# Kernel tuning notes

Measured on AMD Instinct MI355X. Metric: run time of the kernel, lower is better.

Reference implementation:

```python
import jax, jax.numpy as jnp
import numpy as np

B, T, IN, H, L, P = 512, 512, 1, 100, 4, 0.5  # batch, seq, input, hidden, layers, dropout


def setup_inputs() -> dict:
    key = jax.random.key(0)
    ks = jax.random.split(key, 12)
    k = 1.0 / np.sqrt(H)  # torch nn.LSTM init scale
    u = lambda kk, shape: jax.random.uniform(kk, shape, jnp.float32, -k, k)
    inp = {
        "x": jax.random.normal(ks[0], (B, T, IN), jnp.float32),
        "W_ih0": u(ks[1], (4 * H, IN)),          # layer 0 input weights
        "W_ih_rest": u(ks[2], (L - 1, 4 * H, H)),  # layers 1..3 input weights
        "W_hh": u(ks[3], (L, 4 * H, H)),
        "b_ih": u(ks[4], (L, 4 * H)),
        "b_hh": u(ks[5], (L, 4 * H)),
        "W_out": u(ks[6], (1, H)),
        "b_out": u(ks[7], (1,)),
        # inter-layer dropout keep-masks (torch applies dropout to outputs of layers 0..L-2)
        "drop_masks": jax.random.bernoulli(ks[8], 1.0 - P, (L - 1, B, T, H)).astype(jnp.float32),
    }
    return inp


def _lstm_layer(seq, Wih, Whh, b):
    # seq: [T, B, in_dim]; returns [T, B, H]. PyTorch gate order: i, f, g, o.
    h0 = jnp.zeros((seq.shape[1], Whh.shape[-1]), seq.dtype)

    def step(carry, xt):
        h, c = carry
        gates = xt @ Wih.T + h @ Whh.T + b  # [B, 4H]
        i, f, g, o = jnp.split(gates, 4, axis=-1)
        c = jax.nn.sigmoid(f) * c + jax.nn.sigmoid(i) * jnp.tanh(g)
        h = jax.nn.sigmoid(o) * jnp.tanh(c)
        return (h, c), h

    _, hs = jax.lax.scan(step, (h0, h0), seq)
    return hs


def reference(x, W_ih0, W_ih_rest, W_hh, b_ih, b_hh, W_out, b_out, drop_masks):
    scale = 1.0 / (1.0 - P)
    seq = jnp.swapaxes(x, 0, 1)  # [T, B, IN] (batch_first -> time-major)
    seq = _lstm_layer(seq, W_ih0, W_hh[0], b_ih[0] + b_hh[0])
    for l in range(1, L):
        seq = seq * (jnp.swapaxes(drop_masks[l - 1], 0, 1) * scale)
        seq = _lstm_layer(seq, W_ih_rest[l - 1], W_hh[l], b_ih[l] + b_hh[l])
    last = seq[-1]  # [B, H] == lstm_out[:, -1]
    return last @ W_out.T + b_out  # [B, 1]
```

## Files before the change

### kernel.cpp

```cpp
#include <hip/hip_runtime.h>
#include <cstdint>
#include <cstddef>

#define BB 512
#define TT 512
#define HH 100
#define G4 400

template<bool IS_L0, bool WRITE_DROP>
__global__ __launch_bounds__(448, 1)
void rec_kernel(const float* __restrict__ x,
                const float* __restrict__ xc,
                const float* __restrict__ Whh_l,
                const float* __restrict__ Wih0,
                const float* __restrict__ bih_l,
                const float* __restrict__ bhh_l,
                const float* __restrict__ dmask_l,
                float* __restrict__ hdrop,
                float* __restrict__ st_h,
                float* __restrict__ st_c)
{
    __shared__ float sh[G4 * HH];

    const int tid  = threadIdx.x;
    const int e    = (tid < 224) ? 0 : 1;
    const int off  = tid - e * 224;
    const int j    = off >> 1;
    const int role = off & 1;
    const bool active = (j < HH);
    const int jc   = active ? j : (HH - 1);
    const int r0   = role * 100 + jc;
    const int r1   = r0 + 200;
    const int b    = blockIdx.x * 2 + e;

    {
        const float4* src = (const float4*)Whh_l;
        float4* dst = (float4*)sh;
        for (int i = tid; i < G4 * HH / 4; i += 448) dst[i] = src[i];
    }
    __syncthreads();

    float4 wf0[25], wf1[25];
    {
        const float4* s0 = (const float4*)&sh[r0 * HH];
        const float4* s1 = (const float4*)&sh[r1 * HH];
        #pragma unroll
        for (int m = 0; m < 25; ++m) { wf0[m] = s0[m]; wf1[m] = s1[m]; }
    }
    __syncthreads();

    for (int i = tid; i < G4 * HH; i += 448) sh[i] = 0.f;

    float wx0 = 0.f, wx1 = 0.f, bs0 = 0.f, bs1 = 0.f;
    if (IS_L0) {
        wx0 = Wih0[r0];  bs0 = bih_l[r0] + bhh_l[r0];
        wx1 = Wih0[r1];  bs1 = bih_l[r1] + bhh_l[r1];
    }

    const bool isB = (role == 1);
    float c2 = 0.f, hlast = 0.f;

    __syncthreads();

    float gin0 = 0.f, gin1 = 0.f, xv = 0.f, mk = 0.f;
    if (IS_L0) {
        xv = x[(size_t)b * TT];
    } else {
        gin0 = xc[(size_t)b * G4 + r0];
        gin1 = xc[(size_t)b * G4 + r1];
    }
    if (WRITE_DROP && isB && active) mk = dmask_l[(size_t)b * TT * HH + jc];

    int cur = 0;
    for (int t = 0; t < TT; ++t) {
        const int tn = (t + 1 < TT) ? (t + 1) : t;

        float nxv = 0.f, ngin0 = 0.f, ngin1 = 0.f, nmk = 0.f;
        if (IS_L0) {
            nxv = x[(size_t)b * TT + tn];
        } else {
            const size_t base = (size_t)tn * (BB * G4) + (size_t)b * G4;
            ngin0 = xc[base + r0];
            ngin1 = xc[base + r1];
        }
        if (WRITE_DROP && isB && active)
            nmk = dmask_l[((size_t)b * TT + tn) * HH + jc];

        if (IS_L0) {
            gin0 = fmaf(xv, wx0, bs0);
            gin1 = fmaf(xv, wx1, bs1);
        }

        float a0 = 0.f, a0b = 0.f, a1 = 0.f, a1b = 0.f;
        {
            const float4* hp = (const float4*)&sh[cur * 224 + e * 112];
            #pragma unroll
            for (int m = 0; m < 25; ++m) {
                const float4 hv = hp[m];
                a0  = fmaf(wf0[m].x, hv.x, a0);
                a0b = fmaf(wf0[m].y, hv.y, a0b);
                a0  = fmaf(wf0[m].z, hv.z, a0);
                a0b = fmaf(wf0[m].w, hv.w, a0b);
                a1  = fmaf(wf1[m].x, hv.x, a1);
                a1b = fmaf(wf1[m].y, hv.y, a1b);
                a1  = fmaf(wf1[m].z, hv.z, a1);
                a1b = fmaf(wf1[m].w, hv.w, a1b);
            }
        }
        const float pre0 = a0 + a0b + gin0;
        const float pre1 = a1 + a1b + gin1;

        const float s0 = 1.f / (1.f + __expf(-pre0));
        const float E1 = __expf(isB ? (-pre1) : (pre1 + pre1));
        const float rr = 1.f / (1.f + E1);
        const float s1 = isB ? rr : fmaf(-2.f, rr, 1.f);

        const float pv   = s0 * s1;
        const float recv = __shfl_xor(pv, 1);

        const int nxt = cur ^ 1;
        if (isB) {
            c2 = fmaf(s0, c2, recv);
            const float Ec = __expf(c2 + c2);
            const float th = 1.f - 2.f / (Ec + 1.f);
            const float h  = s1 * th;
            hlast = h;
            if (active) {
                sh[nxt * 224 + e * 112 + j] = h;
                if (WRITE_DROP)
                    hdrop[((size_t)t * BB + b) * HH + j] = h * mk * 2.f;
            }
        }
        __syncthreads();
        cur = nxt;
        gin0 = ngin0; gin1 = ngin1; xv = nxv; mk = nmk;
    }

    if (isB && active) {
        st_h[(size_t)b * HH + j] = hlast;
        st_c[(size_t)b * HH + j] = c2;
    }
}

__global__ __launch_bounds__(256, 2)
void xc_gemm(const float* __restrict__ A,
             const float* __restrict__ W,
             const float* __restrict__ bih_l,
             const float* __restrict__ bhh_l,
             float* __restrict__ xc)
{
    __shared__ float At[HH][132];
    __shared__ float Bt[HH][68];

    const int tid = threadIdx.x;
    const int n0  = blockIdx.x * 64;
    const size_t m0 = (size_t)blockIdx.y * 128;

    for (int s = tid; s < 128 * 25; s += 256) {
        const int r = s / 25, kq = s - r * 25;
        const float4 v = *(const float4*)&A[(m0 + r) * HH + kq * 4];
        At[kq * 4 + 0][r] = v.x; At[kq * 4 + 1][r] = v.y;
        At[kq * 4 + 2][r] = v.z; At[kq * 4 + 3][r] = v.w;
    }
    for (int s = tid; s < 64 * 25; s += 256) {
        const int r = s / 25, kq = s - r * 25;
        const int col = n0 + r;
        float4 v = {0.f, 0.f, 0.f, 0.f};
        if (col < G4) v = *(const float4*)&W[(size_t)col * HH + kq * 4];
        Bt[kq * 4 + 0][r] = v.x; Bt[kq * 4 + 1][r] = v.y;
        Bt[kq * 4 + 2][r] = v.z; Bt[kq * 4 + 3][r] = v.w;
    }
    __syncthreads();

    const int tx = tid & 15;
    const int ty = tid >> 4;
    float acc[8][4];
    #pragma unroll
    for (int i = 0; i < 8; ++i)
        #pragma unroll
        for (int j = 0; j < 4; ++j) acc[i][j] = 0.f;

    #pragma unroll 4
    for (int k = 0; k < HH; ++k) {
        const float4 a0 = *(const float4*)&At[k][ty * 8];
        const float4 a1 = *(const float4*)&At[k][ty * 8 + 4];
        const float4 bv = *(const float4*)&Bt[k][tx * 4];
        const float av[8] = {a0.x, a0.y, a0.z, a0.w, a1.x, a1.y, a1.z, a1.w};
        #pragma unroll
        for (int i = 0; i < 8; ++i) {
            acc[i][0] = fmaf(av[i], bv.x, acc[i][0]);
            acc[i][1] = fmaf(av[i], bv.y, acc[i][1]);
            acc[i][2] = fmaf(av[i], bv.z, acc[i][2]);
            acc[i][3] = fmaf(av[i], bv.w, acc[i][3]);
        }
    }

    const int col = n0 + tx * 4;
    if (col < G4) {
        const float4 u = *(const float4*)&bih_l[col];
        const float4 v = *(const float4*)&bhh_l[col];
        const float4 bias = {u.x + v.x, u.y + v.y, u.z + v.z, u.w + v.w};
        #pragma unroll
        for (int i = 0; i < 8; ++i) {
            const size_t r = m0 + ty * 8 + i;
            float4 o = {acc[i][0] + bias.x, acc[i][1] + bias.y,
                        acc[i][2] + bias.z, acc[i][3] + bias.w};
            *(float4*)&xc[r * G4 + col] = o;
        }
    }
}

__global__ __launch_bounds__(256)
void out_kernel(const float* __restrict__ st_h3,
                const float* __restrict__ Wout,
                const float* __restrict__ bout,
                float* __restrict__ out)
{
    const int b = blockIdx.x * 256 + threadIdx.x;
    if (b < BB) {
        float sum = bout[0];
        #pragma unroll 4
        for (int k = 0; k < HH; ++k)
            sum = fmaf(st_h3[(size_t)b * HH + k], Wout[k], sum);
        out[b] = sum;
    }
}

extern "C" void kernel_launch(void* const* d_in, const int* in_sizes, int n_in,
                              void* d_out, int out_size, void* d_ws, size_t ws_size,
                              hipStream_t stream)
{
    const float* x     = (const float*)d_in[0];
    const float* Wih0  = (const float*)d_in[1];
    const float* WihR  = (const float*)d_in[2];
    const float* Whh   = (const float*)d_in[3];
    const float* bih   = (const float*)d_in[4];
    const float* bhh   = (const float*)d_in[5];
    const float* Wout  = (const float*)d_in[6];
    const float* bout  = (const float*)d_in[7];
    const float* dmask = (const float*)d_in[8];
    float* out = (float*)d_out;

    float* ws    = (float*)d_ws;
    float* xcb   = ws;
    float* hdrop = xcb + (size_t)TT * BB * G4;
    float* sth   = hdrop + (size_t)TT * BB * HH;
    float* stc   = sth + (size_t)4 * BB * HH;

    const dim3 rgrid(BB / 2), rblk(448);
    const dim3 ggrid(7, (TT * BB) / 128), gblk(256);

    rec_kernel<true, true><<<rgrid, rblk, 0, stream>>>(
        x, nullptr, Whh, Wih0, bih, bhh, dmask,
        hdrop, sth, stc);
    for (int l = 1; l < 4; ++l) {
        xc_gemm<<<ggrid, gblk, 0, stream>>>(
            hdrop, WihR + (size_t)(l - 1) * G4 * HH,
            bih + l * G4, bhh + l * G4, xcb);
        if (l < 3) {
            rec_kernel<false, true><<<rgrid, rblk, 0, stream>>>(
                nullptr, xcb, Whh + (size_t)l * G4 * HH,
                nullptr, nullptr, nullptr,
                dmask + (size_t)l * BB * TT * HH,
                hdrop, sth + (size_t)l * BB * HH, stc + (size_t)l * BB * HH);
        } else {
            rec_kernel<false, false><<<rgrid, rblk, 0, stream>>>(
                nullptr, xcb, Whh + (size_t)l * G4 * HH,
                nullptr, nullptr, nullptr,
                nullptr,
                nullptr, sth + (size_t)l * BB * HH, stc + (size_t)l * BB * HH);
        }
    }
    out_kernel<<<dim3(2), dim3(256), 0, stream>>>(sth + (size_t)3 * BB * HH, Wout, bout, out);
}
```

Before: 3.578 ms.

## Split hidden-dot over thread pairs with interleaved batch h buffer

The recurrent kernel now assigns four threads per hidden unit: two gate pairs times two batch elements. Each thread holds half of the K range of weights and computes partial dot products for both batch rows, then exchanges halves via shuffle. The h state is interleaved [j][batch] in a tiny shared buffer so one float4 load serves both batches. Weights load directly from global rather than staging through a large shared array. This halves per-thread FMA chain length per step and cuts LDS footprint, at the cost of an extra shuffle per step.

```diff
diff --git a/kernel.cpp b/kernel.cpp
--- a/kernel.cpp
+++ b/kernel.cpp
@@ -20,123 +20,130 @@
                 float* __restrict__ st_h,
                 float* __restrict__ st_c)
 {
-    __shared__ float sh[G4 * HH];
+    __shared__ float hbuf[2][112][2];
 
     const int tid  = threadIdx.x;
-    const int e    = (tid < 224) ? 0 : 1;
-    const int off  = tid - e * 224;
-    const int j    = off >> 1;
-    const int role = off & 1;
+    const int j    = tid >> 2;
+    const int g    = tid & 3;
+    const int pair = g >> 1;
+    const int par  = g & 1;
     const bool active = (j < HH);
     const int jc   = active ? j : (HH - 1);
-    const int r0   = role * 100 + jc;
-    const int r1   = r0 + 200;
-    const int b    = blockIdx.x * 2 + e;
-
+    const int rA   = pair * 100 + jc;
+    const int rB   = rA + 200;
+    const int b    = blockIdx.x * 2 + par;
+    const bool isFO = (pair == 1);
+
+    float wA[52], wB[52];
     {
-        const float4* src = (const float4*)Whh_l;
-        float4* dst = (float4*)sh;
-        for (int i = tid; i < G4 * HH / 4; i += 448) dst[i] = src[i];
-    }
+        const int kb = par * 48;
+        const float4* pa = (const float4*)(Whh_l + (size_t)rA * HH + kb);
+        const float4* pb = (const float4*)(Whh_l + (size_t)rB * HH + kb);
+        const int nf = 12 + par;
+        #pragma unroll
+        for (int m = 0; m < 13; ++m) {
+            float4 va = {0.f, 0.f, 0.f, 0.f};
+            float4 vb = {0.f, 0.f, 0.f, 0.f};
+            if (m < nf) { va = pa[m]; vb = pb[m]; }
+            wA[4 * m + 0] = va.x; wA[4 * m + 1] = va.y;
+            wA[4 * m + 2] = va.z; wA[4 * m + 3] = va.w;
+            wB[4 * m + 0] = vb.x; wB[4 * m + 1] = vb.y;
+            wB[4 * m + 2] = vb.z; wB[4 * m + 3] = vb.w;
+        }
+    }
+
+    float wxA = 0.f, wxB = 0.f, bsA = 0.f, bsB = 0.f;
+    if (IS_L0) {
+        wxA = Wih0[rA];  bsA = bih_l[rA] + bhh_l[rA];
+        wxB = Wih0[rB];  bsB = bih_l[rB] + bhh_l[rB];
+    }
+
+    ((float*)hbuf)[tid] = 0.f;
+
+    float c2 = 0.f, hlast = 0.f;
     __syncthreads();
 
-    float4 wf0[25], wf1[25];
-    {
-        const float4* s0 = (const float4*)&sh[r0 * HH];
-        const float4* s1 = (const float4*)&sh[r1 * HH];
-        #pragma unroll
-        for (int m = 0; m < 25; ++m) { wf0[m] = s0[m]; wf1[m] = s1[m]; }
-    }
-    __syncthreads();
-
-    for (int i = tid; i < G4 * HH; i += 448) sh[i] = 0.f;
-
-    float wx0 = 0.f, wx1 = 0.f, bs0 = 0.f, bs1 = 0.f;
-    if (IS_L0) {
-        wx0 = Wih0[r0];  bs0 = bih_l[r0] + bhh_l[r0];
-        wx1 = Wih0[r1];  bs1 = bih_l[r1] + bhh_l[r1];
-    }
-
-    const bool isB = (role == 1);
-    float c2 = 0.f, hlast = 0.f;
-
-    __syncthreads();
-
-    float gin0 = 0.f, gin1 = 0.f, xv = 0.f, mk = 0.f;
+    float ginA = 0.f, ginB = 0.f, xv = 0.f, mk = 0.f;
     if (IS_L0) {
         xv = x[(size_t)b * TT];
     } else {
-        gin0 = xc[(size_t)b * G4 + r0];
-        gin1 = xc[(size_t)b * G4 + r1];
-    }
-    if (WRITE_DROP && isB && active) mk = dmask_l[(size_t)b * TT * HH + jc];
+        ginA = xc[(size_t)b * G4 + rA];
+        ginB = xc[(size_t)b * G4 + rB];
+    }
+    if (WRITE_DROP && isFO && active) mk = dmask_l[(size_t)b * TT * HH + jc];
 
     int cur = 0;
     for (int t = 0; t < TT; ++t) {
         const int tn = (t + 1 < TT) ? (t + 1) : t;
 
-        float nxv = 0.f, ngin0 = 0.f, ngin1 = 0.f, nmk = 0.f;
+        float nxv = 0.f, nginA = 0.f, nginB = 0.f, nmk = 0.f;
         if (IS_L0) {
             nxv = x[(size_t)b * TT + tn];
         } else {
             const size_t base = (size_t)tn * (BB * G4) + (size_t)b * G4;
-            ngin0 = xc[base + r0];
-            ngin1 = xc[base + r1];
-        }
-        if (WRITE_DROP && isB && active)
+            nginA = xc[base + rA];
+            nginB = xc[base + rB];
+        }
+        if (WRITE_DROP && isFO && active)
             nmk = dmask_l[((size_t)b * TT + tn) * HH + jc];
 
         if (IS_L0) {
-            gin0 = fmaf(xv, wx0, bs0);
-            gin1 = fmaf(xv, wx1, bs1);
-        }
-
-        float a0 = 0.f, a0b = 0.f, a1 = 0.f, a1b = 0.f;
+            ginA = fmaf(xv, wxA, bsA);
+            ginB = fmaf(xv, wxB, bsB);
+        }
+
+        float aA0 = 0.f, aA1 = 0.f, aB0 = 0.f, aB1 = 0.f;
         {
-            const float4* hp = (const float4*)&sh[cur * 224 + e * 112];
+            const float4* hp4 = (const float4*)&hbuf[cur][par * 48][0];
             #pragma unroll
-            for (int m = 0; m < 25; ++m) {
-                const float4 hv = hp[m];
-                a0  = fmaf(wf0[m].x, hv.x, a0);
-                a0b = fmaf(wf0[m].y, hv.y, a0b);
-                a0  = fmaf(wf0[m].z, hv.z, a0);
-                a0b = fmaf(wf0[m].w, hv.w, a0b);
-                a1  = fmaf(wf1[m].x, hv.x, a1);
-                a1b = fmaf(wf1[m].y, hv.y, a1b);
-                a1  = fmaf(wf1[m].z, hv.z, a1);
-                a1b = fmaf(wf1[m].w, hv.w, a1b);
+            for (int m = 0; m < 26; ++m) {
+                const float4 hv = hp4[m];
+                aA0 = fmaf(wA[2 * m],     hv.x, aA0);
+                aA1 = fmaf(wA[2 * m],     hv.y, aA1);
+                aB0 = fmaf(wB[2 * m],     hv.x, aB0);
+                aB1 = fmaf(wB[2 * m],     hv.y, aB1);
+                aA0 = fmaf(wA[2 * m + 1], hv.z, aA0);
+                aA1 = fmaf(wA[2 * m + 1], hv.w, aA1);
+                aB0 = fmaf(wB[2 * m + 1], hv.z, aB0);
+                aB1 = fmaf(wB[2 * m + 1], hv.w, aB1);
             }
         }
-        const float pre0 = a0 + a0b + gin0;
-        const float pre1 = a1 + a1b + gin1;
-
-        const float s0 = 1.f / (1.f + __expf(-pre0));
-        const float E1 = __expf(isB ? (-pre1) : (pre1 + pre1));
-        const float rr = 1.f / (1.f + E1);
-        const float s1 = isB ? rr : fmaf(-2.f, rr, 1.f);
-
-        const float pv   = s0 * s1;
-        const float recv = __shfl_xor(pv, 1);
+
+        const float sendA = par ? aA0 : aA1;
+        const float keepA = par ? aA1 : aA0;
+        const float totA  = keepA + __shfl_xor(sendA, 1) + ginA;
+        const float sendB = par ? aB0 : aB1;
+        const float keepB = par ? aB1 : aB0;
+        const float totB  = keepB + __shfl_xor(sendB, 1) + ginB;
+
+        const float eA   = __expf(-totA);
+        const float sA   = 1.f / (1.f + eA);
+        const float eB   = __expf(isFO ? (-totB) : (totB + totB));
+        const float rB_  = 1.f / (1.f + eB);
+        const float actB = isFO ? rB_ : fmaf(-2.f, rB_, 1.f);
+
+        const float ship  = sA * actB;
+        const float recvP = __shfl_xor(ship, 2);
 
         const int nxt = cur ^ 1;
-        if (isB) {
-            c2 = fmaf(s0, c2, recv);
+        if (isFO) {
+            c2 = fmaf(sA, c2, recvP);
             const float Ec = __expf(c2 + c2);
             const float th = 1.f - 2.f / (Ec + 1.f);
-            const float h  = s1 * th;
+            const float h  = actB * th;
             hlast = h;
             if (active) {
-                sh[nxt * 224 + e * 112 + j] = h;
+                hbuf[nxt][j][par] = h;
                 if (WRITE_DROP)
                     hdrop[((size_t)t * BB + b) * HH + j] = h * mk * 2.f;
             }
         }
         __syncthreads();
         cur = nxt;
-        gin0 = ngin0; gin1 = ngin1; xv = nxv; mk = nmk;
-    }
-
-    if (isB && active) {
+        ginA = nginA; ginB = nginB; xv = nxv; mk = nmk;
+    }
+
+    if (isFO && active) {
         st_h[(size_t)b * HH + j] = hlast;
         st_c[(size_t)b * HH + j] = c2;
     }
@@ -178,7 +185,7 @@
     #pragma unroll
     for (int i = 0; i < 8; ++i)
         #pragma unroll
-        for (int j = 0; j < 4; ++j) acc[i][j] = 0.f;
+        for (int jj = 0; jj < 4; ++jj) acc[i][jj] = 0.f;
 
     #pragma unroll 4
     for (int k = 0; k < HH; ++k) {
```

Measured after the change: 3.751 ms. 1.05x slower.

## Split recurrent matvec over 8 lanes per hidden unit with shuffle reductions

Applied to the files above, without the earlier changes.

Reworks the per-timestep recurrent kernel so each hidden unit is handled by 8 threads (4 gates' K-slices × 2 batches). Each thread keeps a 16-wide slice of all four gate rows in registers and reduces partial sums with warp shuffles. Weights now load straight from global memory, and the large shared weight staging buffer becomes a small interleaved h buffer. Gate activations are combined via shuffles instead of a two-role split. The block grows to 832 threads, so each step runs a shorter serial FMA chain but adds shuffle traffic and a larger barrier.

```diff
diff --git a/kernel.cpp b/kernel.cpp
--- a/kernel.cpp
+++ b/kernel.cpp
@@ -8,7 +8,7 @@
 #define G4 400
 
 template<bool IS_L0, bool WRITE_DROP>
-__global__ __launch_bounds__(448, 1)
+__global__ __launch_bounds__(832, 1)
 void rec_kernel(const float* __restrict__ x,
                 const float* __restrict__ xc,
                 const float* __restrict__ Whh_l,
@@ -20,125 +20,171 @@
                 float* __restrict__ st_h,
                 float* __restrict__ st_c)
 {
-    __shared__ float sh[G4 * HH];
-
-    const int tid  = threadIdx.x;
-    const int e    = (tid < 224) ? 0 : 1;
-    const int off  = tid - e * 224;
-    const int j    = off >> 1;
-    const int role = off & 1;
-    const bool active = (j < HH);
-    const int jc   = active ? j : (HH - 1);
-    const int r0   = role * 100 + jc;
-    const int r1   = r0 + 200;
-    const int b    = blockIdx.x * 2 + e;
-
+    __shared__ float hbuf[2][8][36];
+
+    const int tid = threadIdx.x;
+    const int u   = tid >> 3;
+    const int s   = tid & 7;
+    const bool uok = (u < HH);
+    const int uc  = uok ? u : (HH - 1);
+    const int g   = s >> 1;
+    const int e   = s & 1;
+    const int row = g * HH + uc;
+    const int b   = blockIdx.x * 2 + e;
+    const bool hOwn = (g == 1) && uok;
+    const bool isg  = (g == 2);
+
+    float w[4][16];
     {
-        const float4* src = (const float4*)Whh_l;
-        float4* dst = (float4*)sh;
-        for (int i = tid; i < G4 * HH / 4; i += 448) dst[i] = src[i];
-    }
+        const int k0 = 16 * s;
+        #pragma unroll
+        for (int gg = 0; gg < 4; ++gg) {
+            const float* wrow = Whh_l + (size_t)(gg * HH + uc) * HH;
+            #pragma unroll
+            for (int q = 0; q < 4; ++q) {
+                const int gk = k0 + 4 * q;
+                if (gk + 3 < HH) {
+                    const float4 v = *(const float4*)(wrow + gk);
+                    w[gg][4*q+0] = v.x; w[gg][4*q+1] = v.y;
+                    w[gg][4*q+2] = v.z; w[gg][4*q+3] = v.w;
+                } else {
+                    #pragma unroll
+                    for (int i = 0; i < 4; ++i)
+                        w[gg][4*q+i] = (gk + i < HH) ? wrow[gk + i] : 0.f;
+                }
+            }
+        }
+    }
+
+    float wx = 0.f, bs = 0.f;
+    if (IS_L0) { wx = Wih0[row]; bs = bih_l[row] + bhh_l[row]; }
+
+    for (int i = tid; i < 2 * 8 * 36; i += 832) ((float*)hbuf)[i] = 0.f;
+
+    float c2 = 0.f, hlast = 0.f;
     __syncthreads();
 
-    float4 wf0[25], wf1[25];
-    {
-        const float4* s0 = (const float4*)&sh[r0 * HH];
-        const float4* s1 = (const float4*)&sh[r1 * HH];
-        #pragma unroll
-        for (int m = 0; m < 25; ++m) { wf0[m] = s0[m]; wf1[m] = s1[m]; }
-    }
-    __syncthreads();
-
-    for (int i = tid; i < G4 * HH; i += 448) sh[i] = 0.f;
-
-    float wx0 = 0.f, wx1 = 0.f, bs0 = 0.f, bs1 = 0.f;
-    if (IS_L0) {
-        wx0 = Wih0[r0];  bs0 = bih_l[r0] + bhh_l[r0];
-        wx1 = Wih0[r1];  bs1 = bih_l[r1] + bhh_l[r1];
-    }
-
-    const bool isB = (role == 1);
-    float c2 = 0.f, hlast = 0.f;
-
-    __syncthreads();
-
-    float gin0 = 0.f, gin1 = 0.f, xv = 0.f, mk = 0.f;
-    if (IS_L0) {
-        xv = x[(size_t)b * TT];
-    } else {
-        gin0 = xc[(size_t)b * G4 + r0];
-        gin1 = xc[(size_t)b * G4 + r1];
-    }
-    if (WRITE_DROP && isB && active) mk = dmask_l[(size_t)b * TT * HH + jc];
+    const float* pxc = xc ? (xc + (size_t)b * G4 + row) : nullptr;
+    const float* pdm = dmask_l ? (dmask_l + (size_t)b * TT * HH + uc) : nullptr;
+    const float* px  = x ? (x + (size_t)b * TT) : nullptr;
+    float gin = 0.f, xv = 0.f, mk = 0.f;
+    if (IS_L0) xv = px[0];
+    else       gin = pxc[0];
+    if (WRITE_DROP && hOwn) mk = pdm[0];
 
     int cur = 0;
     for (int t = 0; t < TT; ++t) {
-        const int tn = (t + 1 < TT) ? (t + 1) : t;
-
-        float nxv = 0.f, ngin0 = 0.f, ngin1 = 0.f, nmk = 0.f;
-        if (IS_L0) {
-            nxv = x[(size_t)b * TT + tn];
-        } else {
-            const size_t base = (size_t)tn * (BB * G4) + (size_t)b * G4;
-            ngin0 = xc[base + r0];
-            ngin1 = xc[base + r1];
-        }
-        if (WRITE_DROP && isB && active)
-            nmk = dmask_l[((size_t)b * TT + tn) * HH + jc];
-
-        if (IS_L0) {
-            gin0 = fmaf(xv, wx0, bs0);
-            gin1 = fmaf(xv, wx1, bs1);
-        }
-
-        float a0 = 0.f, a0b = 0.f, a1 = 0.f, a1b = 0.f;
+        const bool last = (t + 1 == TT);
+        const float* nxc = (!IS_L0 && !last) ? pxc + (size_t)BB * G4 : pxc;
+        const float* ndm = (WRITE_DROP && hOwn && !last) ? pdm + HH : pdm;
+        const float* npx = (IS_L0 && !last) ? px + 1 : px;
+
+        float nxv = 0.f, ngin = 0.f, nmk = 0.f;
+        if (IS_L0) nxv = npx[0];
+        else       ngin = nxc[0];
+        if (WRITE_DROP && hOwn) nmk = ndm[0];
+
+        if (IS_L0) gin = fmaf(xv, wx, bs);
+
+        float acc[4][2];
+        #pragma unroll
+        for (int gg = 0; gg < 4; ++gg) { acc[gg][0] = 0.f; acc[gg][1] = 0.f; }
         {
-            const float4* hp = (const float4*)&sh[cur * 224 + e * 112];
-            #pragma unroll
-            for (int m = 0; m < 25; ++m) {
-                const float4 hv = hp[m];
-                a0  = fmaf(wf0[m].x, hv.x, a0);
-                a0b = fmaf(wf0[m].y, hv.y, a0b);
-                a0  = fmaf(wf0[m].z, hv.z, a0);
-                a0b = fmaf(wf0[m].w, hv.w, a0b);
-                a1  = fmaf(wf1[m].x, hv.x, a1);
-                a1b = fmaf(wf1[m].y, hv.y, a1b);
-                a1  = fmaf(wf1[m].z, hv.z, a1);
-                a1b = fmaf(wf1[m].w, hv.w, a1b);
+            const float4* hp = (const float4*)&hbuf[cur][s][0];
+            {
+                const float4 h0 = hp[0], h1 = hp[1], h2 = hp[2], h3 = hp[3];
+                #pragma unroll
+                for (int gg = 0; gg < 4; ++gg) {
+                    acc[gg][0] = fmaf(w[gg][0], h0.x, acc[gg][0]);
+                    acc[gg][1] = fmaf(w[gg][0], h0.y, acc[gg][1]);
+                    acc[gg][0] = fmaf(w[gg][1], h0.z, acc[gg][0]);
+                    acc[gg][1] = fmaf(w[gg][1], h0.w, acc[gg][1]);
+                    acc[gg][0] = fmaf(w[gg][2], h1.x, acc[gg][0]);
+                    acc[gg][1] = fmaf(w[gg][2], h1.y, acc[gg][1]);
+                    acc[gg][0] = fmaf(w[gg][3], h1.z, acc[gg][0]);
+                    acc[gg][1] = fmaf(w[gg][3], h1.w, acc[gg][1]);
+                    acc[gg][0] = fmaf(w[gg][4], h2.x, acc[gg][0]);
+                    acc[gg][1] = fmaf(w[gg][4], h2.y, acc[gg][1]);
+                    acc[gg][0] = fmaf(w[gg][5], h2.z, acc[gg][0]);
+                    acc[gg][1] = fmaf(w[gg][5], h2.w, acc[gg][1]);
+                    acc[gg][0] = fmaf(w[gg][6], h3.x, acc[gg][0]);
+                    acc[gg][1] = fmaf(w[gg][6], h3.y, acc[gg][1]);
+                    acc[gg][0] = fmaf(w[gg][7], h3.z, acc[gg][0]);
+                    acc[gg][1] = fmaf(w[gg][7], h3.w, acc[gg][1]);
+                }
             }
-        }
-        const float pre0 = a0 + a0b + gin0;
-        const float pre1 = a1 + a1b + gin1;
-
-        const float s0 = 1.f / (1.f + __expf(-pre0));
-        const float E1 = __expf(isB ? (-pre1) : (pre1 + pre1));
-        const float rr = 1.f / (1.f + E1);
-        const float s1 = isB ? rr : fmaf(-2.f, rr, 1.f);
-
-        const float pv   = s0 * s1;
-        const float recv = __shfl_xor(pv, 1);
+            {
+                const float4 h0 = hp[4], h1 = hp[5], h2 = hp[6], h3 = hp[7];
+                #pragma unroll
+                for (int gg = 0; gg < 4; ++gg) {
+                    acc[gg][0] = fmaf(w[gg][ 8], h0.x, acc[gg][0]);
+                    acc[gg][1] = fmaf(w[gg][ 8], h0.y, acc[gg][1]);
+                    acc[gg][0] = fmaf(w[gg][ 9], h0.z, acc[gg][0]);
+                    acc[gg][1] = fmaf(w[gg][ 9], h0.w, acc[gg][1]);
+                    acc[gg][0] = fmaf(w[gg][10], h1.x, acc[gg][0]);
+                    acc[gg][1] = fmaf(w[gg][10], h1.y, acc[gg][1]);
+                    acc[gg][0] = fmaf(w[gg][11], h1.z, acc[gg][0]);
+                    acc[gg][1] = fmaf(w[gg][11], h1.w, acc[gg][1]);
+                    acc[gg][0] = fmaf(w[gg][12], h2.x, acc[gg][0]);
+                    acc[gg][1] = fmaf(w[gg][12], h2.y, acc[gg][1]);
+                    acc[gg][0] = fmaf(w[gg][13], h2.z, acc[gg][0]);
+                    acc[gg][1] = fmaf(w[gg][13], h2.w, acc[gg][1]);
+                    acc[gg][0] = fmaf(w[gg][14], h3.x, acc[gg][0]);
+                    acc[gg][1] = fmaf(w[gg][14], h3.y, acc[gg][1]);
+                    acc[gg][0] = fmaf(w[gg][15], h3.z, acc[gg][0]);
+                    acc[gg][1] = fmaf(w[gg][15], h3.w, acc[gg][1]);
+                }
+            }
+        }
+
+        float r1_0, r1_1, r1_2, r1_3;
+        {
+            float m0 = e ? acc[0][1] : acc[0][0], o0 = e ? acc[0][0] : acc[0][1];
+            float m1 = e ? acc[1][1] : acc[1][0], o1 = e ? acc[1][0] : acc[1][1];
+            float m2 = e ? acc[2][1] : acc[2][0], o2 = e ? acc[2][0] : acc[2][1];
+            float m3 = e ? acc[3][1] : acc[3][0], o3 = e ? acc[3][0] : acc[3][1];
+            r1_0 = m0 + __shfl_xor(o0, 1);
+            r1_1 = m1 + __shfl_xor(o1, 1);
+            r1_2 = m2 + __shfl_xor(o2, 1);
+            r1_3 = m3 + __shfl_xor(o3, 1);
+        }
+        const bool gb0 = ((s >> 1) & 1) != 0;
+        float r2_0 = gb0 ? r1_1 : r1_0, r2_0o = gb0 ? r1_0 : r1_1;
+        float r2_1 = gb0 ? r1_3 : r1_2, r2_1o = gb0 ? r1_2 : r1_3;
+        r2_0 += __shfl_xor(r2_0o, 2);
+        r2_1 += __shfl_xor(r2_1o, 2);
+        const bool gb1 = ((s >> 2) & 1) != 0;
+        float m3v = gb1 ? r2_1 : r2_0, o3v = gb1 ? r2_0 : r2_1;
+        const float tot = m3v + __shfl_xor(o3v, 4) + gin;
+
+        const float E1  = __expf(isg ? (tot + tot) : (-tot));
+        const float rr  = 1.f / (1.f + E1);
+        const float act = isg ? fmaf(-2.f, rr, 1.f) : rr;
+
+        const float recvP = __shfl_xor(act, 4);
+        const float prod = act * recvP;
+        const float ig   = __shfl_xor(prod, 2);
 
         const int nxt = cur ^ 1;
-        if (isB) {
-            c2 = fmaf(s0, c2, recv);
+        if (hOwn) {
+            c2 = fmaf(act, c2, ig);
             const float Ec = __expf(c2 + c2);
             const float th = 1.f - 2.f / (Ec + 1.f);
-            const float h  = s1 * th;
+            const float h  = recvP * th;
             hlast = h;
-            if (active) {
-                sh[nxt * 224 + e * 112 + j] = h;
-                if (WRITE_DROP)
-                    hdrop[((size_t)t * BB + b) * HH + j] = h * mk * 2.f;
-            }
+            hbuf[nxt][u >> 4][(u & 15) * 2 + e] = h;
+            if (WRITE_DROP)
+                hdrop[((size_t)t * BB + b) * HH + u] = h * mk * 2.f;
         }
         __syncthreads();
         cur = nxt;
-        gin0 = ngin0; gin1 = ngin1; xv = nxv; mk = nmk;
-    }
-
-    if (isB && active) {
-        st_h[(size_t)b * HH + j] = hlast;
-        st_c[(size_t)b * HH + j] = c2;
+        gin = ngin; xv = nxv; mk = nmk;
+        pxc = nxc; pdm = ndm; px = npx;
+    }
+
+    if (hOwn) {
+        st_h[(size_t)b * HH + u] = hlast;
+        st_c[(size_t)b * HH + u] = c2;
     }
 }
 
@@ -178,7 +224,7 @@
     #pragma unroll
     for (int i = 0; i < 8; ++i)
         #pragma unroll
-        for (int j = 0; j < 4; ++j) acc[i][j] = 0.f;
+        for (int jj = 0; jj < 4; ++jj) acc[i][jj] = 0.f;
 
     #pragma unroll 4
     for (int k = 0; k < HH; ++k) {
@@ -247,7 +293,7 @@
     float* sth   = hdrop + (size_t)TT * BB * HH;
     float* stc   = sth + (size_t)4 * BB * HH;
 
-    const dim3 rgrid(BB / 2), rblk(448);
+    const dim3 rgrid(BB / 2), rblk(832);
     const dim3 ggrid(7, (TT * BB) / 128), gblk(256);
 
     rec_kernel<true, true><<<rgrid, rblk, 0, stream>>>(
```

New measurement: 3.938 ms. +10.1%, slower.

## Split recurrent matvec over K across 8 lanes with shuffle reduction

Applied to the files above, without the earlier changes.

Restructures the recurrent LSTM kernel so each group of 8 lanes owns two hidden units across all four gates, with each lane holding a 16-wide K slice of the weights and both batch rows interleaved in a small shared h buffer. Partial dot products are combined with a butterfly of xor-shuffles, and gate activations are exchanged between lanes by shuffles. This shrinks the per-thread serial dot-product chain and the shared-memory h reads per step, at the cost of extra shuffle and select operations per timestep and pointer-increment addressing.

```diff
diff --git a/kernel.cpp b/kernel.cpp
--- a/kernel.cpp
+++ b/kernel.cpp
@@ -20,125 +20,190 @@
                 float* __restrict__ st_h,
                 float* __restrict__ st_c)
 {
-    __shared__ float sh[G4 * HH];
-
-    const int tid  = threadIdx.x;
-    const int e    = (tid < 224) ? 0 : 1;
-    const int off  = tid - e * 224;
-    const int j    = off >> 1;
-    const int role = off & 1;
-    const bool active = (j < HH);
-    const int jc   = active ? j : (HH - 1);
-    const int r0   = role * 100 + jc;
-    const int r1   = r0 + 200;
-    const int b    = blockIdx.x * 2 + e;
+    __shared__ float Wst[G4 * HH];
+    __shared__ float hbuf[2][8][36];
+
+    const int tid = threadIdx.x;
+    const int p   = tid >> 3;
+    const int s   = tid & 7;
+    const int g   = s >> 1;
+    const int e   = s & 1;
+    const bool active = (p < 50);
+    const int pc  = active ? p : 49;
+    const int b   = blockIdx.x * 2 + e;
+    const bool isF = (g == 1);
+    const bool isG = (g == 2);
 
     {
         const float4* src = (const float4*)Whh_l;
-        float4* dst = (float4*)sh;
+        float4* dst = (float4*)Wst;
         for (int i = tid; i < G4 * HH / 4; i += 448) dst[i] = src[i];
     }
     __syncthreads();
 
-    float4 wf0[25], wf1[25];
+    float w[4][2][16];
+    #pragma unroll
+    for (int gg = 0; gg < 4; ++gg) {
+        #pragma unroll
+        for (int du = 0; du < 2; ++du) {
+            const float* rowp = &Wst[(size_t)(gg * HH + 2 * pc + du) * HH];
+            #pragma unroll
+            for (int q = 0; q < 4; ++q) {
+                const int gk = 16 * s + 4 * q;
+                float4 v = {0.f, 0.f, 0.f, 0.f};
+                if (gk < HH) v = *(const float4*)(rowp + gk);
+                w[gg][du][4*q+0] = v.x; w[gg][du][4*q+1] = v.y;
+                w[gg][du][4*q+2] = v.z; w[gg][du][4*q+3] = v.w;
+            }
+        }
+    }
+    __syncthreads();
+
     {
-        const float4* s0 = (const float4*)&sh[r0 * HH];
-        const float4* s1 = (const float4*)&sh[r1 * HH];
-        #pragma unroll
-        for (int m = 0; m < 25; ++m) { wf0[m] = s0[m]; wf1[m] = s1[m]; }
-    }
+        float4* dst = (float4*)Wst;
+        const float4 z = {0.f, 0.f, 0.f, 0.f};
+        for (int i = tid; i < G4 * HH / 4; i += 448) dst[i] = z;
+    }
+    for (int i = tid; i < 2 * 8 * 36; i += 448) ((float*)hbuf)[i] = 0.f;
+
+    float wx[2] = {0.f, 0.f}, bsv[2] = {0.f, 0.f};
+    if (IS_L0) {
+        #pragma unroll
+        for (int du = 0; du < 2; ++du) {
+            const int row = g * HH + 2 * pc + du;
+            wx[du]  = Wih0[row];
+            bsv[du] = bih_l[row] + bhh_l[row];
+        }
+    }
+
+    float c2[2] = {0.f, 0.f}, hl[2] = {0.f, 0.f};
     __syncthreads();
 
-    for (int i = tid; i < G4 * HH; i += 448) sh[i] = 0.f;
-
-    float wx0 = 0.f, wx1 = 0.f, bs0 = 0.f, bs1 = 0.f;
-    if (IS_L0) {
-        wx0 = Wih0[r0];  bs0 = bih_l[r0] + bhh_l[r0];
-        wx1 = Wih0[r1];  bs1 = bih_l[r1] + bhh_l[r1];
-    }
-
-    const bool isB = (role == 1);
-    float c2 = 0.f, hlast = 0.f;
-
-    __syncthreads();
-
-    float gin0 = 0.f, gin1 = 0.f, xv = 0.f, mk = 0.f;
-    if (IS_L0) {
-        xv = x[(size_t)b * TT];
-    } else {
-        gin0 = xc[(size_t)b * G4 + r0];
-        gin1 = xc[(size_t)b * G4 + r1];
-    }
-    if (WRITE_DROP && isB && active) mk = dmask_l[(size_t)b * TT * HH + jc];
+    const float* pA0 = xc ? (xc + (size_t)b * G4 + g * HH + 2 * pc + 0) : nullptr;
+    const float* pA1 = xc ? (xc + (size_t)b * G4 + g * HH + 2 * pc + 1) : nullptr;
+    const float* pm0 = dmask_l ? (dmask_l + (size_t)b * TT * HH + 2 * pc + 0) : nullptr;
+    const float* pm1 = dmask_l ? (dmask_l + (size_t)b * TT * HH + 2 * pc + 1) : nullptr;
+    const float* px  = x ? (x + (size_t)b * TT) : nullptr;
+
+    float gin0 = 0.f, gin1 = 0.f, xv = 0.f, mk0 = 0.f, mk1 = 0.f;
+    if (IS_L0) xv = px[0];
+    else { gin0 = pA0[0]; gin1 = pA1[0]; }
+    if (WRITE_DROP && isF && active) { mk0 = pm0[0]; mk1 = pm1[0]; }
 
     int cur = 0;
     for (int t = 0; t < TT; ++t) {
-        const int tn = (t + 1 < TT) ? (t + 1) : t;
-
-        float nxv = 0.f, ngin0 = 0.f, ngin1 = 0.f, nmk = 0.f;
+        const bool last = (t + 1 == TT);
+        const float* nA0 = (!IS_L0 && !last) ? pA0 + (size_t)BB * G4 : pA0;
+        const float* nA1 = (!IS_L0 && !last) ? pA1 + (size_t)BB * G4 : pA1;
+        const float* nm0 = (WRITE_DROP && !last) ? pm0 + HH : pm0;
+        const float* nm1 = (WRITE_DROP && !last) ? pm1 + HH : pm1;
+        const float* npx = (IS_L0 && !last) ? px + 1 : px;
+
+        float nxv = 0.f, ngin0 = 0.f, ngin1 = 0.f, nmk0 = 0.f, nmk1 = 0.f;
+        if (IS_L0) nxv = npx[0];
+        else { ngin0 = nA0[0]; ngin1 = nA1[0]; }
+        if (WRITE_DROP && isF && active) { nmk0 = nm0[0]; nmk1 = nm1[0]; }
+
         if (IS_L0) {
-            nxv = x[(size_t)b * TT + tn];
-        } else {
-            const size_t base = (size_t)tn * (BB * G4) + (size_t)b * G4;
-            ngin0 = xc[base + r0];
-            ngin1 = xc[base + r1];
-        }
-        if (WRITE_DROP && isB && active)
-            nmk = dmask_l[((size_t)b * TT + tn) * HH + jc];
-
-        if (IS_L0) {
-            gin0 = fmaf(xv, wx0, bs0);
-            gin1 = fmaf(xv, wx1, bs1);
-        }
-
-        float a0 = 0.f, a0b = 0.f, a1 = 0.f, a1b = 0.f;
+            gin0 = fmaf(xv, wx[0], bsv[0]);
+            gin1 = fmaf(xv, wx[1], bsv[1]);
+        }
+
+        float acc[4][2][2];
+        #pragma unroll
+        for (int gg = 0; gg < 4; ++gg)
+            #pragma unroll
+            for (int du = 0; du < 2; ++du)
+                { acc[gg][du][0] = 0.f; acc[gg][du][1] = 0.f; }
         {
-            const float4* hp = (const float4*)&sh[cur * 224 + e * 112];
-            #pragma unroll
-            for (int m = 0; m < 25; ++m) {
-                const float4 hv = hp[m];
-                a0  = fmaf(wf0[m].x, hv.x, a0);
-                a0b = fmaf(wf0[m].y, hv.y, a0b);
-                a0  = fmaf(wf0[m].z, hv.z, a0);
-                a0b = fmaf(wf0[m].w, hv.w, a0b);
-                a1  = fmaf(wf1[m].x, hv.x, a1);
-                a1b = fmaf(wf1[m].y, hv.y, a1b);
-                a1  = fmaf(wf1[m].z, hv.z, a1);
-                a1b = fmaf(wf1[m].w, hv.w, a1b);
-            }
-        }
-        const float pre0 = a0 + a0b + gin0;
-        const float pre1 = a1 + a1b + gin1;
-
-        const float s0 = 1.f / (1.f + __expf(-pre0));
-        const float E1 = __expf(isB ? (-pre1) : (pre1 + pre1));
-        const float rr = 1.f / (1.f + E1);
-        const float s1 = isB ? rr : fmaf(-2.f, rr, 1.f);
-
-        const float pv   = s0 * s1;
-        const float recv = __shfl_xor(pv, 1);
+            const float4* hp = (const float4*)&hbuf[cur][s][0];
+            #pragma unroll
+            for (int i = 0; i < 8; ++i) {
+                const float4 hv = hp[i];
+                #pragma unroll
+                for (int gg = 0; gg < 4; ++gg) {
+                    #pragma unroll
+                    for (int du = 0; du < 2; ++du) {
+                        acc[gg][du][0] = fmaf(w[gg][du][2*i],   hv.x, acc[gg][du][0]);
+                        acc[gg][du][1] = fmaf(w[gg][du][2*i],   hv.y, acc[gg][du][1]);
+                        acc[gg][du][0] = fmaf(w[gg][du][2*i+1], hv.z, acc[gg][du][0]);
+                        acc[gg][du][1] = fmaf(w[gg][du][2*i+1], hv.w, acc[gg][du][1]);
+                    }
+                }
+            }
+        }
+
+        float v1[4][2];
+        #pragma unroll
+        for (int gg = 0; gg < 4; ++gg)
+            #pragma unroll
+            for (int du = 0; du < 2; ++du) {
+                const float m = e ? acc[gg][du][1] : acc[gg][du][0];
+                const float o = e ? acc[gg][du][0] : acc[gg][du][1];
+                v1[gg][du] = m + __shfl_xor(o, 1);
+            }
+        const int bt0 = (s >> 1) & 1;
+        float v2[2][2];
+        #pragma unroll
+        for (int gh = 0; gh < 2; ++gh)
+            #pragma unroll
+            for (int du = 0; du < 2; ++du) {
+                const float m = bt0 ? v1[gh*2+1][du] : v1[gh*2+0][du];
+                const float o = bt0 ? v1[gh*2+0][du] : v1[gh*2+1][du];
+                v2[gh][du] = m + __shfl_xor(o, 2);
+            }
+        const int bt1 = (s >> 2) & 1;
+        float tot[2];
+        #pragma unroll
+        for (int du = 0; du < 2; ++du) {
+            const float m = bt1 ? v2[1][du] : v2[0][du];
+            const float o = bt1 ? v2[0][du] : v2[1][du];
+            tot[du] = m + __shfl_xor(o, 4);
+        }
+        tot[0] += gin0;
+        tot[1] += gin1;
+
+        float act[2], rc4[2], igv[2];
+        #pragma unroll
+        for (int du = 0; du < 2; ++du) {
+            const float E  = __expf(isG ? (tot[du] + tot[du]) : (-tot[du]));
+            const float rr = 1.f / (1.f + E);
+            act[du] = isG ? fmaf(-2.f, rr, 1.f) : rr;
+        }
+        #pragma unroll
+        for (int du = 0; du < 2; ++du) rc4[du] = __shfl_xor(act[du], 4);
+        #pragma unroll
+        for (int du = 0; du < 2; ++du) igv[du] = __shfl_xor(act[du] * rc4[du], 2);
 
         const int nxt = cur ^ 1;
-        if (isB) {
-            c2 = fmaf(s0, c2, recv);
-            const float Ec = __expf(c2 + c2);
-            const float th = 1.f - 2.f / (Ec + 1.f);
-            const float h  = s1 * th;
-            hlast = h;
-            if (active) {
-                sh[nxt * 224 + e * 112 + j] = h;
-                if (WRITE_DROP)
-                    hdrop[((size_t)t * BB + b) * HH + j] = h * mk * 2.f;
+        if (isF && active) {
+            #pragma unroll
+            for (int du = 0; du < 2; ++du) {
+                c2[du] = fmaf(act[du], c2[du], igv[du]);
+                const float Ec = __expf(c2[du] + c2[du]);
+                const float th = 1.f - 2.f / (Ec + 1.f);
+                const float h  = rc4[du] * th;
+                hl[du] = h;
+                const int u = 2 * pc + du;
+                hbuf[nxt][u >> 4][(u & 15) * 2 + e] = h;
+            }
+            if (WRITE_DROP) {
+                hdrop[((size_t)t * BB + b) * HH + 2 * pc + 0] = hl[0] * mk0 * 2.f;
+                hdrop[((size_t)t * BB + b) * HH + 2 * pc + 1] = hl[1] * mk1 * 2.f;
             }
         }
         __syncthreads();
         cur = nxt;
-        gin0 = ngin0; gin1 = ngin1; xv = nxv; mk = nmk;
-    }
-
-    if (isB && active) {
-        st_h[(size_t)b * HH + j] = hlast;
-        st_c[(size_t)b * HH + j] = c2;
+        gin0 = ngin0; gin1 = ngin1; xv = nxv; mk0 = nmk0; mk1 = nmk1;
+        pA0 = nA0; pA1 = nA1; pm0 = nm0; pm1 = nm1; px = npx;
+    }
+
+    if (isF && active) {
+        #pragma unroll
+        for (int du = 0; du < 2; ++du) {
+            st_h[(size_t)b * HH + 2 * pc + du] = hl[du];
+            st_c[(size_t)b * HH + 2 * pc + du] = c2[du];
+        }
     }
 }
 
@@ -178,7 +243,7 @@
     #pragma unroll
     for (int i = 0; i < 8; ++i)
         #pragma unroll
-        for (int j = 0; j < 4; ++j) acc[i][j] = 0.f;
+        for (int jj = 0; jj < 4; ++jj) acc[i][jj] = 0.f;
 
     #pragma unroll 4
     for (int k = 0; k < HH; ++k) {
```

Result: slower. 4.174 ms (+16.7%).
